# Performance work log

Hardware: AMD Instinct MI355X
Metric: run time of the kernel (lower is better)

## Reference

```python
import jax, jax.numpy as jnp
import numpy as np

B, C, H, W = 4, 64, 64, 64

def _conv1x1(x, w, b):
    # Conv2d(k=1): y[b,o,h,w] = sum_c x[b,c,h,w]*w[o,c] + b[o]
    return jnp.einsum('bchw,oc->bohw', x, w) + b[None, :, None, None]

def setup_inputs() -> dict:
    key = jax.random.key(0)
    ks = jax.random.split(key, 8)
    s = 1.0 / np.sqrt(C)
    return {
        'v1': jax.random.normal(ks[0], (B, C, H, W), jnp.float32),
        'v2': jax.random.normal(ks[1], (B, C, H, W), jnp.float32),
        'wq': jax.random.normal(ks[2], (C, C), jnp.float32) * s,
        'bq': jax.random.normal(ks[3], (C,), jnp.float32) * 0.01,
        'wk': jax.random.normal(ks[4], (C, C), jnp.float32) * s,
        'bk': jax.random.normal(ks[5], (C,), jnp.float32) * 0.01,
        'wv': jax.random.normal(ks[6], (C, C), jnp.float32) * s,
        'bv': jax.random.normal(ks[7], (C,), jnp.float32) * 0.01,
    }

def reference(v1, v2, wq, bq, wk, bk, wv, bv):
    q = _conv1x1(v1, wq, bq)   # (B,C,H,W)
    k = _conv1x1(v2, wk, bk)
    v = _conv1x1(v2, wv, bv)
    b, c, h, w = q.shape
    n = c * h                   # tokens = C*H, feature dim = W (matches torch view)
    qf = q.reshape(b, n, w)
    kf = k.reshape(b, n, w)
    vf = v.reshape(b, n, w)
    scores = jnp.einsum('bnw,bmw->bnm', qf, kf)   # (B, N, N)
    attn = jax.nn.softmax(scores, axis=-1)
    out = jnp.einsum('bnm,bmw->bnw', attn, vf)
    return out.reshape(v1.shape)
```

## Files before the change

kernel.cpp:

```cpp
#include <hip/hip_runtime.h>


#define Bn 4
#define Cc 64
#define HW 4096
#define Nn 4096
#define Dd 64
#define TS (Bn * Nn * Dd)
#define LOG2E 1.44269504088896340736f

typedef _Float16 f16;
typedef _Float16 f16x8 __attribute__((ext_vector_type(8)));
typedef _Float16 f16x4 __attribute__((ext_vector_type(4)));
typedef float f32x4 __attribute__((ext_vector_type(4)));

__device__ __forceinline__ int swz(int row, int col) {
    return row * 64 + (col ^ ((row & 7) << 3));
}

__device__ __forceinline__ void gl_lds16(const f16* g, f16* l) {
    __builtin_amdgcn_global_load_lds(
        (const __attribute__((address_space(1))) unsigned int*)g,
        (__attribute__((address_space(3))) unsigned int*)l, 16, 0, 0);
}

__global__ __launch_bounds__(256) void qkv_conv(
    const float* __restrict__ v1, const float* __restrict__ v2,
    const float* __restrict__ wq, const float* __restrict__ bq,
    const float* __restrict__ wk, const float* __restrict__ bk,
    const float* __restrict__ wv, const float* __restrict__ bv,
    f16* __restrict__ Qh, f16* __restrict__ Kh, f16* __restrict__ Vh)
{
    const int t    = threadIdx.x;
    const int lane = t & 63;
    const int og   = __builtin_amdgcn_readfirstlane(t >> 6);
    const int b    = blockIdx.y;
    const int p    = blockIdx.x * 64 + lane;
    const int z    = blockIdx.z;
    const int zt   = z >> 1;
    const int ch0  = (z & 1) * 32 + og * 8;

    const float* w    = (zt == 0) ? wq : (zt == 1) ? wk : wv;
    const float* bias = (zt == 0) ? bq : (zt == 1) ? bk : bv;
    const float* x    = ((zt == 0) ? v1 : v2) + (size_t)b * (Cc * HW) + p;

    float acc[8];
    #pragma unroll
    for (int j = 0; j < 8; ++j) acc[j] = bias[ch0 + j];
    #pragma unroll 16
    for (int c = 0; c < 64; ++c) {
        float xc = x[c * HW];
        #pragma unroll
        for (int j = 0; j < 8; ++j)
            acc[j] = fmaf(w[(ch0 + j) * 64 + c], xc, acc[j]);
    }

    f16* dst = (zt == 0) ? Qh : (zt == 1) ? Kh : Vh;
    const float scale = (zt == 0) ? LOG2E : 1.0f;
    #pragma unroll
    for (int j = 0; j < 8; ++j) {
        size_t idx = (size_t)b * (Nn * Dd) + (size_t)(ch0 + j) * 4096 + p;
        dst[idx] = (f16)(acc[j] * scale);
    }
}

__global__ __launch_bounds__(256) void vtrans(const f16* __restrict__ Vh,
                                              f16* __restrict__ Vt)
{
    __shared__ f16 tile[64][72];
    const int t  = threadIdx.x;
    const int n0 = blockIdx.x * 64;
    const int b  = blockIdx.y;
    for (int i = t; i < 4096; i += 256) {
        int r = i >> 6, c = i & 63;
        tile[r][c] = Vh[(size_t)b * (Nn * Dd) + (size_t)(n0 + r) * 64 + c];
    }
    __syncthreads();
    for (int i = t; i < 4096; i += 256) {
        int w = i >> 6, n = i & 63;
        Vt[(size_t)b * (Dd * Nn) + (size_t)w * Nn + n0 + n] = tile[n][w];
    }
}

__global__ __launch_bounds__(256, 3) void attn(
    const f16* __restrict__ Qhg, const f16* __restrict__ Khg,
    const f16* __restrict__ Vtg,
    float* __restrict__ out, f16* __restrict__ Opart, float2* __restrict__ ml)
{
    __shared__ __align__(16) f16 KT[2][4096];
    __shared__ __align__(16) f16 VT[2][4096];
    __shared__ __align__(16) f16 Pt[8192];

    const int t    = threadIdx.x;
    const int lane = t & 63, wvi = t >> 6;
    const int g = lane >> 4, c = lane & 15;
    const int rl = lane >> 3, cg = lane & 7;
    const int b  = blockIdx.z;
    const int sp = blockIdx.y;
    const int S  = gridDim.y;
    const int n0 = blockIdx.x * 128;
    const int keysPerSplit = Nn / S;
    const int nTiles = keysPerSplit / 64;
    const int kbase = sp * keysPerSplit;

    const f16* Kb = Khg + (size_t)b * (Nn * Dd);
    const f16* Vb = Vtg + (size_t)b * (Dd * Nn);

    f16x8 qbh[2][2];
    #pragma unroll
    for (int qf = 0; qf < 2; ++qf) {
        const int qrow = n0 + wvi * 32 + qf * 16 + c;
        const f16* qhp = Qhg + ((size_t)b * Nn + qrow) * 64;
        #pragma unroll
        for (int ks = 0; ks < 2; ++ks)
            qbh[qf][ks] = *(const f16x8*)(qhp + ks * 32 + g * 8);
    }

    float m_run[2] = {-1e30f, -1e30f}, lpart[2] = {0.f, 0.f};
    f32x4 of[2][4];
    #pragma unroll
    for (int qf = 0; qf < 2; ++qf)
        #pragma unroll
        for (int nf = 0; nf < 4; ++nf)
            #pragma unroll
            for (int r = 0; r < 4; ++r) of[qf][nf][r] = 0.f;

    {
        const int k0 = kbase;
        #pragma unroll
        for (int i = 0; i < 2; ++i) {
            const int row = wvi * 16 + i * 8 + rl;
            const int gc  = (cg ^ (row & 7)) * 8;
            gl_lds16(Kb + (size_t)(k0 + row) * 64 + gc,
                     &KT[0][(wvi * 16 + i * 8) * 64]);
            gl_lds16(Vb + (size_t)row * Nn + k0 + gc,
                     &VT[0][(wvi * 16 + i * 8) * 64]);
        }
    }
    __syncthreads();
    int cur = 0;

    for (int kt = 0; kt < nTiles; ++kt) {
        if (kt + 1 < nTiles) {
            const int k0n = kbase + (kt + 1) * 64;
            #pragma unroll
            for (int i = 0; i < 2; ++i) {
                const int row = wvi * 16 + i * 8 + rl;
                const int gc  = (cg ^ (row & 7)) * 8;
                gl_lds16(Kb + (size_t)(k0n + row) * 64 + gc,
                         &KT[cur ^ 1][(wvi * 16 + i * 8) * 64]);
                gl_lds16(Vb + (size_t)row * Nn + k0n + gc,
                         &VT[cur ^ 1][(wvi * 16 + i * 8) * 64]);
            }
        }

        const f16* KTc = KT[cur];
        const f16* VTc = VT[cur];

        f32x4 accS[2][4];
        #pragma unroll
        for (int qf = 0; qf < 2; ++qf)
            #pragma unroll
            for (int fm = 0; fm < 4; ++fm)
                #pragma unroll
                for (int r = 0; r < 4; ++r) accS[qf][fm][r] = 0.f;
        #pragma unroll
        for (int fm = 0; fm < 4; ++fm) {
            const int key = fm * 16 + c;
            f16x8 kh0 = *(const f16x8*)(KTc + swz(key, g * 8));
            f16x8 kh1 = *(const f16x8*)(KTc + swz(key, 32 + g * 8));
            #pragma unroll
            for (int qf = 0; qf < 2; ++qf) {
                accS[qf][fm] = __builtin_amdgcn_mfma_f32_16x16x32_f16(kh0, qbh[qf][0], accS[qf][fm], 0, 0, 0);
                accS[qf][fm] = __builtin_amdgcn_mfma_f32_16x16x32_f16(kh1, qbh[qf][1], accS[qf][fm], 0, 0, 0);
            }
        }

        #pragma unroll
        for (int qf = 0; qf < 2; ++qf) {
            float m0 = fmaxf(fmaxf(accS[qf][0][0], accS[qf][0][1]),
                             fmaxf(accS[qf][0][2], accS[qf][0][3]));
            float m1 = fmaxf(fmaxf(accS[qf][1][0], accS[qf][1][1]),
                             fmaxf(accS[qf][1][2], accS[qf][1][3]));
            float m2 = fmaxf(fmaxf(accS[qf][2][0], accS[qf][2][1]),
                             fmaxf(accS[qf][2][2], accS[qf][2][3]));
            float m3 = fmaxf(fmaxf(accS[qf][3][0], accS[qf][3][1]),
                             fmaxf(accS[qf][3][2], accS[qf][3][3]));
            float tmax = fmaxf(fmaxf(m0, m1), fmaxf(m2, m3));
            tmax = fmaxf(tmax, __shfl_xor(tmax, 16));
            tmax = fmaxf(tmax, __shfl_xor(tmax, 32));
            if (!__all(tmax <= m_run[qf] + 8.f)) {
                const float mnew = fmaxf(m_run[qf], tmax);
                const float corr = exp2f(m_run[qf] - mnew);
                lpart[qf] *= corr;
                #pragma unroll
                for (int r = 0; r < 4; ++r) {
                    float cr = __shfl(corr, g * 4 + r);
                    #pragma unroll
                    for (int nf = 0; nf < 4; ++nf) of[qf][nf][r] *= cr;
                }
                m_run[qf] = mnew;
            }
            float s01 = 0.f, s23 = 0.f;
            #pragma unroll
            for (int fm = 0; fm < 4; ++fm)
                #pragma unroll
                for (int r = 0; r < 4; ++r) {
                    float pp = exp2f(accS[qf][fm][r] - m_run[qf]);
                    accS[qf][fm][r] = pp;
                    if (fm < 2) s01 += pp; else s23 += pp;
                }
            lpart[qf] += s01 + s23;

            const int prow = wvi * 32 + qf * 16 + c;
            #pragma unroll
            for (int fm = 0; fm < 4; ++fm) {
                f16x4 pk;
                #pragma unroll
                for (int r = 0; r < 4; ++r) pk[r] = (f16)accS[qf][fm][r];
                *(f16x4*)(Pt + swz(prow, fm * 16 + g * 4)) = pk;
            }
        }

        #pragma unroll
        for (int ks = 0; ks < 2; ++ks) {
            f16x8 pa0 = *(const f16x8*)(Pt + swz(wvi * 32 + c,      ks * 32 + g * 8));
            f16x8 pa1 = *(const f16x8*)(Pt + swz(wvi * 32 + 16 + c, ks * 32 + g * 8));
            #pragma unroll
            for (int nf = 0; nf < 4; ++nf) {
                f16x8 vb = *(const f16x8*)(VTc + swz(nf * 16 + c, ks * 32 + g * 8));
                of[0][nf] = __builtin_amdgcn_mfma_f32_16x16x32_f16(pa0, vb, of[0][nf], 0, 0, 0);
                of[1][nf] = __builtin_amdgcn_mfma_f32_16x16x32_f16(pa1, vb, of[1][nf], 0, 0, 0);
            }
        }

        __syncthreads();
        cur ^= 1;
    }

    if (S == 1) {
        #pragma unroll
        for (int qf = 0; qf < 2; ++qf) {
            float lr = lpart[qf];
            lr += __shfl_xor(lr, 16);
            lr += __shfl_xor(lr, 32);
            const float linv = 1.0f / lr;
            #pragma unroll
            for (int r = 0; r < 4; ++r) {
                float li = __shfl(linv, g * 4 + r);
                int n = n0 + wvi * 32 + qf * 16 + g * 4 + r;
                #pragma unroll
                for (int nf = 0; nf < 4; ++nf)
                    out[((size_t)b * Nn + n) * 64 + nf * 16 + c] = of[qf][nf][r] * li;
            }
        }
    } else {
        #pragma unroll
        for (int qf = 0; qf < 2; ++qf) {
            float lr = lpart[qf];
            lr += __shfl_xor(lr, 16);
            lr += __shfl_xor(lr, 32);
            const float linv = 1.0f / lr;
            #pragma unroll
            for (int r = 0; r < 4; ++r) {
                float li = __shfl(linv, g * 4 + r);
                int n = n0 + wvi * 32 + qf * 16 + g * 4 + r;
                size_t robase = (((size_t)sp * Bn + b) * Nn + n) * 64;
                #pragma unroll
                for (int nf = 0; nf < 4; ++nf)
                    Opart[robase + nf * 16 + c] = (f16)(of[qf][nf][r] * li);
            }
            if (lane < 16) {
                int n = n0 + wvi * 32 + qf * 16 + c;
                ml[((size_t)sp * Bn + b) * Nn + n] = make_float2(m_run[qf], lr);
            }
        }
    }
}

__global__ __launch_bounds__(256) void combine(
    const f16* __restrict__ Opart, const float2* __restrict__ ml,
    float* __restrict__ out, int S)
{
    const int idx8 = blockIdx.x * 256 + threadIdx.x;
    const int w8 = idx8 & 7;
    const int n  = (idx8 >> 3) & (Nn - 1);
    const int b  = idx8 >> 15;
    float M = -1e30f;
    for (int s = 0; s < S; ++s)
        M = fmaxf(M, ml[((size_t)s * Bn + b) * Nn + n].x);
    float num[8];
    #pragma unroll
    for (int j = 0; j < 8; ++j) num[j] = 0.f;
    float den = 0.f;
    for (int s = 0; s < S; ++s) {
        float2 m2 = ml[((size_t)s * Bn + b) * Nn + n];
        float a = exp2f(m2.x - M) * m2.y;
        f16x8 o8 = *(const f16x8*)(Opart + ((((size_t)s * Bn + b) * Nn + n) << 6) + w8 * 8);
        #pragma unroll
        for (int j = 0; j < 8; ++j) num[j] += a * (float)o8[j];
        den += a;
    }
    const float di = 1.0f / den;
    float* op = out + (((size_t)b * Nn + n) << 6) + w8 * 8;
    float4 lo = make_float4(num[0] * di, num[1] * di, num[2] * di, num[3] * di);
    float4 hi = make_float4(num[4] * di, num[5] * di, num[6] * di, num[7] * di);
    *(float4*)op = lo;
    *(float4*)(op + 4) = hi;
}

extern "C" void kernel_launch(void* const* d_in, const int* in_sizes, int n_in,
                              void* d_out, int out_size, void* d_ws, size_t ws_size,
                              hipStream_t stream)
{
    const float* v1 = (const float*)d_in[0];
    const float* v2 = (const float*)d_in[1];
    const float* wq = (const float*)d_in[2];
    const float* bq = (const float*)d_in[3];
    const float* wk = (const float*)d_in[4];
    const float* bk = (const float*)d_in[5];
    const float* wv = (const float*)d_in[6];
    const float* bv = (const float*)d_in[7];
    float* out = (float*)d_out;

    char* ws = (char*)d_ws;
    const size_t T = (size_t)TS * sizeof(f16);
    f16* Qh = (f16*)(ws + 0 * T);
    f16* Kh = (f16*)(ws + 1 * T);
    f16* Vh = (f16*)(ws + 2 * T);
    f16* Vt = (f16*)(ws + 3 * T);
    const size_t base = 4 * T;
    const size_t opartBytes = (size_t)TS * 2;
    const size_t mlBytes    = (size_t)Bn * Nn * 8;

    int S = 1;
    if      (ws_size >= base + 8 * (opartBytes + mlBytes)) S = 8;
    else if (ws_size >= base + 4 * (opartBytes + mlBytes)) S = 4;
    else if (ws_size >= base + 2 * (opartBytes + mlBytes)) S = 2;

    f16*    Opart = (f16*)(ws + base);
    float2* mlp   = (float2*)(ws + base + (size_t)S * opartBytes);

    qkv_conv<<<dim3(64, 4, 6), 256, 0, stream>>>(v1, v2, wq, bq, wk, bk, wv, bv,
                                                 Qh, Kh, Vh);
    vtrans<<<dim3(64, 4), 256, 0, stream>>>(Vh, Vt);
    attn<<<dim3(32, S, 4), 256, 0, stream>>>(Qh, Kh, Vt, out, Opart, mlp);
    if (S > 1) {
        combine<<<(Bn * Nn * Dd / 8) / 256, 256, 0, stream>>>(Opart, mlp, out, S);
    }
}
```

Measured before the change: 71.34 us.

## Double attention block to 512 threads, 256 queries, single-load K/V staging

The attention kernel now runs 8 waves per block covering 256 query rows, so each K/V tile staged in LDS is reused by twice as many queries. With more threads, every thread issues one global-to-LDS load per tile for K and V instead of two. P is packed to fp16 with the cvt_pkrtz intrinsic, which rounds toward zero instead of to nearest. The cost is half as many blocks in the grid, a larger LDS footprint for P, and a tighter register budget from the 512-thread, 4-block launch bounds.

```diff
diff --git a/kernel.cpp b/kernel.cpp
--- a/kernel.cpp
+++ b/kernel.cpp
@@ -12,6 +12,7 @@
 typedef _Float16 f16;
 typedef _Float16 f16x8 __attribute__((ext_vector_type(8)));
 typedef _Float16 f16x4 __attribute__((ext_vector_type(4)));
+typedef __fp16 fp16x2 __attribute__((ext_vector_type(2)));
 typedef float f32x4 __attribute__((ext_vector_type(4)));
 
 __device__ __forceinline__ int swz(int row, int col) {
@@ -82,27 +83,33 @@
     }
 }
 
-__global__ __launch_bounds__(256, 3) void attn(
+__global__ __launch_bounds__(512, 4) void attn(
     const f16* __restrict__ Qhg, const f16* __restrict__ Khg,
     const f16* __restrict__ Vtg,
     float* __restrict__ out, f16* __restrict__ Opart, float2* __restrict__ ml)
 {
     __shared__ __align__(16) f16 KT[2][4096];
     __shared__ __align__(16) f16 VT[2][4096];
-    __shared__ __align__(16) f16 Pt[8192];
+    __shared__ __align__(16) f16 Pt[16384];
 
     const int t    = threadIdx.x;
     const int lane = t & 63, wvi = t >> 6;
     const int g = lane >> 4, c = lane & 15;
-    const int rl = lane >> 3, cg = lane & 7;
     const int b  = blockIdx.z;
     const int sp = blockIdx.y;
     const int S  = gridDim.y;
-    const int n0 = blockIdx.x * 128;
+    const int n0 = blockIdx.x * 256;
     const int keysPerSplit = Nn / S;
     const int nTiles = keysPerSplit / 64;
     const int kbase = sp * keysPerSplit;
 
+    const int srow = t >> 3;
+    const int gc   = ((t & 7) ^ (srow & 7)) * 8;
+    f16* ldsKdst0 = &KT[0][(wvi * 8) * 64];
+    f16* ldsKdst1 = &KT[1][(wvi * 8) * 64];
+    f16* ldsVdst0 = &VT[0][(wvi * 8) * 64];
+    f16* ldsVdst1 = &VT[1][(wvi * 8) * 64];
+
     const f16* Kb = Khg + (size_t)b * (Nn * Dd);
     const f16* Vb = Vtg + (size_t)b * (Dd * Nn);
 
@@ -125,33 +132,18 @@
             #pragma unroll
             for (int r = 0; r < 4; ++r) of[qf][nf][r] = 0.f;
 
-    {
-        const int k0 = kbase;
-        #pragma unroll
-        for (int i = 0; i < 2; ++i) {
-            const int row = wvi * 16 + i * 8 + rl;
-            const int gc  = (cg ^ (row & 7)) * 8;
-            gl_lds16(Kb + (size_t)(k0 + row) * 64 + gc,
-                     &KT[0][(wvi * 16 + i * 8) * 64]);
-            gl_lds16(Vb + (size_t)row * Nn + k0 + gc,
-                     &VT[0][(wvi * 16 + i * 8) * 64]);
-        }
-    }
+    gl_lds16(Kb + (size_t)(kbase + srow) * 64 + gc, ldsKdst0);
+    gl_lds16(Vb + (size_t)srow * Nn + kbase + gc, ldsVdst0);
     __syncthreads();
     int cur = 0;
 
     for (int kt = 0; kt < nTiles; ++kt) {
         if (kt + 1 < nTiles) {
             const int k0n = kbase + (kt + 1) * 64;
-            #pragma unroll
-            for (int i = 0; i < 2; ++i) {
-                const int row = wvi * 16 + i * 8 + rl;
-                const int gc  = (cg ^ (row & 7)) * 8;
-                gl_lds16(Kb + (size_t)(k0n + row) * 64 + gc,
-                         &KT[cur ^ 1][(wvi * 16 + i * 8) * 64]);
-                gl_lds16(Vb + (size_t)row * Nn + k0n + gc,
-                         &VT[cur ^ 1][(wvi * 16 + i * 8) * 64]);
-            }
+            f16* kd = cur ? ldsKdst0 : ldsKdst1;
+            f16* vd = cur ? ldsVdst0 : ldsVdst1;
+            gl_lds16(Kb + (size_t)(k0n + srow) * 64 + gc, kd);
+            gl_lds16(Vb + (size_t)srow * Nn + k0n + gc, vd);
         }
 
         const f16* KTc = KT[cur];
@@ -215,10 +207,10 @@
             const int prow = wvi * 32 + qf * 16 + c;
             #pragma unroll
             for (int fm = 0; fm < 4; ++fm) {
-                f16x4 pk;
-                #pragma unroll
-                for (int r = 0; r < 4; ++r) pk[r] = (f16)accS[qf][fm][r];
-                *(f16x4*)(Pt + swz(prow, fm * 16 + g * 4)) = pk;
+                union { f16x4 v4; fp16x2 h2[2]; } u;
+                u.h2[0] = __builtin_amdgcn_cvt_pkrtz(accS[qf][fm][0], accS[qf][fm][1]);
+                u.h2[1] = __builtin_amdgcn_cvt_pkrtz(accS[qf][fm][2], accS[qf][fm][3]);
+                *(f16x4*)(Pt + swz(prow, fm * 16 + g * 4)) = u.v4;
             }
         }
 
@@ -344,7 +336,7 @@
     qkv_conv<<<dim3(64, 4, 6), 256, 0, stream>>>(v1, v2, wq, bq, wk, bk, wv, bv,
                                                  Qh, Kh, Vh);
     vtrans<<<dim3(64, 4), 256, 0, stream>>>(Vh, Vt);
-    attn<<<dim3(32, S, 4), 256, 0, stream>>>(Qh, Kh, Vt, out, Opart, mlp);
+    attn<<<dim3(16, S, 4), 512, 0, stream>>>(Qh, Kh, Vt, out, Opart, mlp);
     if (S > 1) {
         combine<<<(Bn * Nn * Dd / 8) / 256, 256, 0, stream>>>(Opart, mlp, out, S);
     }
```

After: 69.62 us. -2.4%, faster.
